# Kernel optimization log

Hardware: AMD Instinct MI355X
Metric: run time of the kernel (lower is better)

The kernel has to match this reference:

```python
import jax, jax.numpy as jnp
import numpy as np

T, H, NH, NKV, HD = 4096, 2048, 16, 2, 256
ROT = 64           # partial_rotary_factor 0.25 * head_dim 256
HALF = ROT // 2    # 32 == sum(mrope_section [11, 11, 10])
BASE = 10_000_000.0
EPS = 1e-6
SCALE = HD ** -0.5


def setup_inputs() -> dict:
    key = jax.random.key(0)
    ks = jax.random.split(key, 8)
    s = 0.02
    return {
        "positions": jnp.sort(jax.random.randint(ks[0], (3, T), 0, 4096), axis=-1),
        "hidden": jax.random.normal(ks[1], (T, H), jnp.float32),
        "Wq": jax.random.normal(ks[2], (H, NH * HD * 2), jnp.float32) * s,
        "Wk": jax.random.normal(ks[3], (H, NKV * HD), jnp.float32) * s,
        "Wv": jax.random.normal(ks[4], (H, NKV * HD), jnp.float32) * s,
        "Wo": jax.random.normal(ks[5], (NH * HD, H), jnp.float32) * s,
        "q_norm_w": jax.random.normal(ks[6], (HD,), jnp.float32) * 0.1,
        "k_norm_w": jax.random.normal(ks[7], (HD,), jnp.float32) * 0.1,
    }


def _rms(x, w):
    # GemmaRMSNorm: x / rms * (1 + w), per-head over last dim
    var = jnp.mean(x * x, axis=-1, keepdims=True)
    return x * jax.lax.rsqrt(var + EPS) * (1.0 + w)


def _rope_tables(positions):
    # interleaved MRoPE: freq j uses position axis j % 3 -> counts [11,11,10]
    inv_freq = BASE ** (-jnp.arange(0, ROT, 2, dtype=jnp.float32) / ROT)  # [HALF]
    axis = jnp.arange(HALF) % 3
    pos = positions[axis, :].astype(jnp.float32)   # [HALF, T]
    freqs = pos.T * inv_freq                       # [T, HALF]
    return jnp.cos(freqs), jnp.sin(freqs)


def _apply_rope(x, cos, sin):
    # x: [T, heads, HD]; rotate first ROT dims (neox half-split), rest pass through
    x1, x2 = x[..., :HALF], x[..., HALF:ROT]
    c, s = cos[:, None, :], sin[:, None, :]
    return jnp.concatenate([x1 * c - x2 * s, x2 * c + x1 * s, x[..., ROT:]], axis=-1)


def reference(positions, hidden, Wq, Wk, Wv, Wo, q_norm_w, k_norm_w):
    qg = (hidden @ Wq).reshape(T, NH, 2 * HD)
    q, gate = qg[..., :HD], qg[..., HD:]          # chunk(2, dim=-1)
    k = (hidden @ Wk).reshape(T, NKV, HD)
    v = (hidden @ Wv).reshape(T, NKV, HD)
    q = _rms(q, q_norm_w)
    k = _rms(k, k_norm_w)
    cos, sin = _rope_tables(positions)
    q = _apply_rope(q, cos, sin)
    k = _apply_rope(k, cos, sin)
    # GQA causal attention: group 16 Q heads over 2 KV heads
    g = NH // NKV
    q4 = q.reshape(T, NKV, g, HD)
    scores = jnp.einsum('qkgd,tkd->kgqt', q4, k) * SCALE   # [NKV, g, T, T]
    mask = jnp.tril(jnp.ones((T, T), dtype=bool))
    scores = jnp.where(mask[None, None], scores, -jnp.inf)
    probs = jax.nn.softmax(scores, axis=-1)
    o = jnp.einsum('kgqt,tkd->qkgd', probs, v).reshape(T, NH, HD)
    o = o * jax.nn.sigmoid(gate)                   # per-head output gating
    return o.reshape(T, NH * HD) @ Wo
```

## Files before the change

kernel.cpp:

```cpp
#include <hip/hip_runtime.h>
#include <hip/hip_bf16.h>


#define T_SZ 4096
#define H_SZ 2048
#define NH_SZ 16
#define NKV_SZ 2
#define HD_SZ 256
#define ATT_SCALE 0.0625f
#define SOFT_M 18.0f
#define EPS_ 1e-6f

typedef __attribute__((ext_vector_type(8))) short bf16x8;
typedef __attribute__((ext_vector_type(4))) float f32x4;

#define MFMA16(a, b, c) __builtin_amdgcn_mfma_f32_16x16x32_bf16((a), (b), (c), 0, 0, 0)

__device__ __forceinline__ void async16(const void* g, void* l) {
  __builtin_amdgcn_global_load_lds((const __attribute__((address_space(1))) void*)g,
                                   (__attribute__((address_space(3))) void*)l,
                                   16, 0, 0);
}

__device__ __forceinline__ float to_f(float x) { return x; }
__device__ __forceinline__ float to_f(__hip_bfloat16 x) { return __bfloat162float(x); }

union BfBits { __hip_bfloat16 h; unsigned short u; };

__device__ __forceinline__ unsigned short bf16_bits(__hip_bfloat16 h) {
  BfBits t; t.h = h; return t.u;
}

__device__ __forceinline__ unsigned pack_hilo(float v) {
  __hip_bfloat16 hi = __float2bfloat16(v);
  float rem = v - __bfloat162float(hi);
  __hip_bfloat16 lo = __float2bfloat16(rem);
  return (unsigned)bf16_bits(hi) | ((unsigned)bf16_bits(lo) << 16);
}

__global__ __launch_bounds__(256) void cast_f32_bf16(const float* __restrict__ in,
                                                     __hip_bfloat16* __restrict__ out,
                                                     int n4) {
  int i = blockIdx.x * 256 + threadIdx.x;
  if (i >= n4) return;
  float4 v = ((const float4*)in)[i];
  union { __hip_bfloat16 h[4]; uint2 u; } t;
  t.h[0] = __float2bfloat16(v.x);
  t.h[1] = __float2bfloat16(v.y);
  t.h[2] = __float2bfloat16(v.z);
  t.h[3] = __float2bfloat16(v.w);
  ((uint2*)out)[i] = t.u;
}

template <typename TIN>
__global__ __launch_bounds__(256) void transpose_cast(const TIN* __restrict__ in,
                                                      __hip_bfloat16* __restrict__ out,
                                                      int R, int C) {
  __shared__ TIN tile[32][33];
  int c0 = blockIdx.x * 32, r0 = blockIdx.y * 32;
  int tx = threadIdx.x & 31, ty = threadIdx.x >> 5;
#pragma unroll
  for (int i = 0; i < 32; i += 8)
    tile[ty + i][tx] = in[(long)(r0 + ty + i) * C + c0 + tx];
  __syncthreads();
#pragma unroll
  for (int i = 0; i < 32; i += 8)
    out[(long)(c0 + ty + i) * R + r0 + tx] = __float2bfloat16(to_f(tile[tx][ty + i]));
}

__global__ __launch_bounds__(256) void transpose_dup(const float* __restrict__ in,
                                                     unsigned* __restrict__ out,
                                                     int R, int C) {
  __shared__ float tile[32][33];
  int c0 = blockIdx.x * 32, r0 = blockIdx.y * 32;
  int tx = threadIdx.x & 31, ty = threadIdx.x >> 5;
#pragma unroll
  for (int i = 0; i < 32; i += 8)
    tile[ty + i][tx] = in[(long)(r0 + ty + i) * C + c0 + tx];
  __syncthreads();
#pragma unroll
  for (int i = 0; i < 32; i += 8) {
    unsigned short b = bf16_bits(__float2bfloat16(tile[tx][ty + i]));
    out[(long)(c0 + ty + i) * R + r0 + tx] = (unsigned)b | ((unsigned)b << 16);
  }
}

__global__ __launch_bounds__(512) void gemm_qg2(const __hip_bfloat16* __restrict__ A,
                                                const __hip_bfloat16* __restrict__ BT,
                                                float* __restrict__ qout,
                                                __hip_bfloat16* __restrict__ gate) {
  __shared__ __align__(16) __hip_bfloat16 As[4][8192];
  __shared__ __align__(16) __hip_bfloat16 Bs[4][8192];
  const int tid = threadIdx.x, wid = tid >> 6, lane = tid & 63;
  const int lo = lane & 15, quad = lane >> 4;
  const int wm = (wid >> 2) * 128, wn = (wid & 3) * 64;
  const int wg = blockIdx.x + blockIdx.y * 8;
  const int xcd = wg & 7, i_ = wg >> 3;
  const long n0 = (long)(xcd * 4 + (i_ & 3)) * 256;
  const long m0 = (long)(i_ >> 2) * 256;
  const int K = 2048;

  const int r0_ = tid >> 2;
  const int kc0 = (tid & 3) ^ ((tid >> 3) & 3);
  const __hip_bfloat16* sA0 = A + (m0 + r0_) * K + kc0 * 8;
  const __hip_bfloat16* sA1 = A + (m0 + r0_ + 128) * K + kc0 * 8;
  const __hip_bfloat16* sB0 = BT + (n0 + r0_) * K + kc0 * 8;
  const __hip_bfloat16* sB1 = BT + (n0 + r0_ + 128) * K + kc0 * 8;

  const int xq = (lo >> 1) & 3;
  const int aoff = (wm + lo) * 32 + ((quad ^ xq) * 8);
  const int boff = (wn + lo) * 32 + ((quad ^ xq) * 8);

  const f32x4 z4 = {0.f, 0.f, 0.f, 0.f};
  f32x4 acc[8][4];
#pragma unroll
  for (int fr = 0; fr < 8; ++fr)
#pragma unroll
    for (int fn = 0; fn < 4; ++fn) acc[fr][fn] = z4;

#define QG_STAGE(buf, kt) do {                                   \
    const int off_ = (kt) * 32;                                  \
    async16(sA0 + off_, &As[buf][tid * 8]);                      \
    async16(sA1 + off_, &As[buf][tid * 8 + 4096]);               \
    async16(sB0 + off_, &Bs[buf][tid * 8]);                      \
    async16(sB1 + off_, &Bs[buf][tid * 8 + 4096]);               \
  } while (0)

#define QG_COMPUTE(buf_) do {                                    \
    bf16x8 af[8], bq[4];                                         \
    _Pragma("unroll")                                            \
    for (int fr = 0; fr < 8; ++fr)                               \
      af[fr] = *(const bf16x8*)(&As[buf_][aoff + fr * 512]);     \
    _Pragma("unroll")                                            \
    for (int fn = 0; fn < 4; ++fn)                               \
      bq[fn] = *(const bf16x8*)(&Bs[buf_][boff + fn * 512]);     \
    __builtin_amdgcn_s_setprio(1);                               \
    _Pragma("unroll")                                            \
    for (int fr = 0; fr < 8; ++fr)                               \
      _Pragma("unroll")                                          \
      for (int fn = 0; fn < 4; ++fn)                             \
        acc[fr][fn] = MFMA16(af[fr], bq[fn], acc[fr][fn]);       \
    __builtin_amdgcn_s_setprio(0);                               \
  } while (0)

  QG_STAGE(0, 0); QG_STAGE(1, 1); QG_STAGE(2, 2);
  for (int kt = 0; kt < 61; ++kt) {
    asm volatile("s_waitcnt vmcnt(8)" ::: "memory");
    __builtin_amdgcn_s_barrier();
    __builtin_amdgcn_sched_barrier(0);
    QG_STAGE((kt + 3) & 3, kt + 3);
    __builtin_amdgcn_sched_barrier(0);
    QG_COMPUTE(kt & 3);
  }
  asm volatile("s_waitcnt vmcnt(8)" ::: "memory");
  __builtin_amdgcn_s_barrier();
  __builtin_amdgcn_sched_barrier(0);
  QG_COMPUTE(1);
  asm volatile("s_waitcnt vmcnt(4)" ::: "memory");
  __builtin_amdgcn_s_barrier();
  __builtin_amdgcn_sched_barrier(0);
  QG_COMPUTE(2);
  asm volatile("s_waitcnt vmcnt(0)" ::: "memory");
  __builtin_amdgcn_s_barrier();
  __builtin_amdgcn_sched_barrier(0);
  QG_COMPUTE(3);
#undef QG_STAGE
#undef QG_COMPUTE

#pragma unroll
  for (int fr = 0; fr < 8; ++fr)
#pragma unroll
    for (int fn = 0; fn < 4; ++fn)
#pragma unroll
      for (int rr = 0; rr < 4; ++rr) {
        long row = m0 + wm + fr * 16 + quad * 4 + rr;
        long col = n0 + wn + fn * 16 + lo;
        int head = (int)(col >> 9), c = (int)(col & 511);
        float v = acc[fr][fn][rr];
        if (c < 256)
          qout[(row * NH_SZ + head) * 256 + c] = v;
        else
          gate[(row * NH_SZ + head) * 256 + (c - 256)] = __float2bfloat16(v);
      }
}

__global__ __launch_bounds__(512) void gemm_out2(const __hip_bfloat16* __restrict__ A,
                                                 const __hip_bfloat16* __restrict__ BT,
                                                 float* __restrict__ C) {
  __shared__ __align__(16) __hip_bfloat16 As[4][8192];
  __shared__ __align__(16) __hip_bfloat16 Bs[4][4096];
  const int tid = threadIdx.x, wid = tid >> 6, lane = tid & 63;
  const int lo = lane & 15, quad = lane >> 4;
  const int wm = (wid >> 1) * 64, wn = (wid & 1) * 64;
  const int wg = blockIdx.x + blockIdx.y * 8;
  const int xcd = wg & 7, i_ = wg >> 3;
  const long n0 = (long)(xcd * 2 + (i_ & 1)) * 128;
  const long m0 = (long)(i_ >> 1) * 256;
  const long Kp = 8192;

  const int rA = tid >> 2, spx = (tid & 3) ^ ((tid >> 2) & 3);
  const __hip_bfloat16* sA0 = A + (m0 + rA) * Kp + spx * 8;
  const __hip_bfloat16* sA1 = A + (m0 + rA + 128) * Kp + spx * 8;
  const __hip_bfloat16* sB0 = BT + (n0 + rA) * Kp + spx * 8;

  const int xa = quad ^ (lo & 3);
  const int aoff = (wm + lo) * 32 + xa * 8;
  const int boff = (wn + lo) * 32 + xa * 8;

  const f32x4 z4 = {0.f, 0.f, 0.f, 0.f};
  f32x4 acc[4][4];
#pragma unroll
  for (int fr = 0; fr < 4; ++fr)
#pragma unroll
    for (int fn = 0; fn < 4; ++fn) acc[fr][fn] = z4;

#define GO_STAGE(buf, kt) do {                                   \
    const long off_ = (long)(kt) * 32;                           \
    async16(sA0 + off_, &As[buf][tid * 8]);                      \
    async16(sA1 + off_, &As[buf][tid * 8 + 4096]);               \
    async16(sB0 + off_, &Bs[buf][tid * 8]);                      \
  } while (0)

#define GO_COMPUTE(buf_) do {                                    \
    bf16x8 af[4], bq[4];                                         \
    _Pragma("unroll")                                            \
    for (int fr = 0; fr < 4; ++fr)                               \
      af[fr] = *(const bf16x8*)(&As[buf_][aoff + fr * 512]);     \
    _Pragma("unroll")                                            \
    for (int fn = 0; fn < 4; ++fn)                               \
      bq[fn] = *(const bf16x8*)(&Bs[buf_][boff + fn * 512]);     \
    __builtin_amdgcn_s_setprio(1);                               \
    _Pragma("unroll")                                            \
    for (int fr = 0; fr < 4; ++fr)                               \
      _Pragma("unroll")                                          \
      for (int fn = 0; fn < 4; ++fn)                             \
        acc[fr][fn] = MFMA16(af[fr], bq[fn], acc[fr][fn]);       \
    __builtin_amdgcn_s_setprio(0);                               \
  } while (0)

  GO_STAGE(0, 0); GO_STAGE(1, 1); GO_STAGE(2, 2);
  for (int kt = 0; kt < 253; ++kt) {
    asm volatile("s_waitcnt vmcnt(6)" ::: "memory");
    __builtin_amdgcn_s_barrier();
    __builtin_amdgcn_sched_barrier(0);
    GO_STAGE((kt + 3) & 3, kt + 3);
    __builtin_amdgcn_sched_barrier(0);
    GO_COMPUTE(kt & 3);
  }
  asm volatile("s_waitcnt vmcnt(6)" ::: "memory");
  __builtin_amdgcn_s_barrier();
  __builtin_amdgcn_sched_barrier(0);
  GO_COMPUTE(1);
  asm volatile("s_waitcnt vmcnt(3)" ::: "memory");
  __builtin_amdgcn_s_barrier();
  __builtin_amdgcn_sched_barrier(0);
  GO_COMPUTE(2);
  asm volatile("s_waitcnt vmcnt(0)" ::: "memory");
  __builtin_amdgcn_s_barrier();
  __builtin_amdgcn_sched_barrier(0);
  GO_COMPUTE(3);
#undef GO_STAGE
#undef GO_COMPUTE

#pragma unroll
  for (int fr = 0; fr < 4; ++fr)
#pragma unroll
    for (int fn = 0; fn < 4; ++fn)
#pragma unroll
      for (int rr = 0; rr < 4; ++rr) {
        long row = m0 + wm + fr * 16 + quad * 4 + rr;
        long col = n0 + wn + fn * 16 + lo;
        C[row * 2048 + col] = acc[fr][fn][rr];
      }
}

__global__ __launch_bounds__(256) void gemm_kv(const __hip_bfloat16* __restrict__ A,
                                               const __hip_bfloat16* __restrict__ BT,
                                               float* __restrict__ kf,
                                               __hip_bfloat16* __restrict__ vraw,
                                               int M, int N, int K) {
  __shared__ __align__(16) __hip_bfloat16 As[128 * 32];
  __shared__ __align__(16) __hip_bfloat16 Bs[128 * 32];
  const int tid = threadIdx.x;
  const int wid = tid >> 6, lane = tid & 63;
  const int lo = lane & 15, quad = lane >> 4;
  const int wq = blockIdx.x + blockIdx.y * 8;
  const int xcd = wq & 7, idx = wq >> 3;
  const long n0 = (long)xcd * 128;
  const long m0 = (long)idx * 128;
  const int wm = (wid >> 1) * 64, wn = (wid & 1) * 64;
  const f32x4 z4 = {0.f, 0.f, 0.f, 0.f};
  f32x4 acc[4][4];
#pragma unroll
  for (int i = 0; i < 4; ++i)
#pragma unroll
    for (int j = 0; j < 4; ++j) acc[i][j] = z4;

  const int cf0 = tid, cf1 = 256 + tid;
  const int r0_ = cf0 >> 2, c0_ = (cf0 & 3) * 8;
  const int r1_ = cf1 >> 2, c1_ = (cf1 & 3) * 8;
  const __hip_bfloat16* a0 = A + (m0 + r0_) * K + c0_;
  const __hip_bfloat16* a1 = A + (m0 + r1_) * K + c1_;
  const __hip_bfloat16* b0 = BT + (n0 + r0_) * K + c0_;
  const __hip_bfloat16* b1 = BT + (n0 + r1_) * K + c1_;

  for (int k0 = 0; k0 < K; k0 += 32) {
    async16(a0 + k0, As + cf0 * 8);
    async16(a1 + k0, As + cf1 * 8);
    async16(b0 + k0, Bs + cf0 * 8);
    async16(b1 + k0, Bs + cf1 * 8);
    __syncthreads();
    bf16x8 af[4], bfv[4];
#pragma unroll
    for (int i = 0; i < 4; ++i)
      af[i] = *(const bf16x8*)(As + (wm + i * 16 + lo) * 32 + quad * 8);
#pragma unroll
    for (int i = 0; i < 4; ++i)
      bfv[i] = *(const bf16x8*)(Bs + (wn + i * 16 + lo) * 32 + quad * 8);
#pragma unroll
    for (int i = 0; i < 4; ++i)
#pragma unroll
      for (int j = 0; j < 4; ++j) acc[i][j] = MFMA16(af[i], bfv[j], acc[i][j]);
    __syncthreads();
  }
#pragma unroll
  for (int i = 0; i < 4; ++i)
#pragma unroll
    for (int j = 0; j < 4; ++j)
#pragma unroll
      for (int r = 0; r < 4; ++r) {
        long row = m0 + wm + i * 16 + quad * 4 + r;
        long col = n0 + wn + j * 16 + lo;
        float v = acc[i][j][r];
        if (col < 512)
          kf[row * 512 + col] = v;
        else
          vraw[row * 512 + (col - 512)] = __float2bfloat16(v);
      }
}

__global__ __launch_bounds__(256) void v_swizzle(const __hip_bfloat16* __restrict__ vraw,
                                                 __hip_bfloat16* __restrict__ vsw) {
  const int ktt = blockIdx.x, kvh = blockIdx.y, tid = threadIdx.x;
  __shared__ __hip_bfloat16 L[64 * 264];
#pragma unroll
  for (int it = 0; it < 8; ++it) {
    int cf = it * 256 + tid;
    int kv = cf >> 5, d0 = (cf & 31) * 8;
    *(uint4*)&L[kv * 264 + d0] =
        *(const uint4*)&vraw[(((long)ktt * 64 + kv) * NKV_SZ + kvh) * 256 + d0];
  }
  __syncthreads();
#pragma unroll
  for (int it = 0; it < 8; ++it) {
    int cf = it * 256 + tid;
    int c = cf >> 8, d = cf & 255;
    union { __hip_bfloat16 h[8]; uint4 u; } t;
#pragma unroll
    for (int e = 0; e < 8; ++e) t.h[e] = L[(c * 8 + e) * 264 + d];
    *(uint4*)&vsw[((long)kvh * 64 + ktt) * 16384 + (long)(c * 256 + d) * 8] = t.u;
  }
}

__global__ __launch_bounds__(256) void norm_rope_wave(float* __restrict__ qbuf,
                                                      const float* __restrict__ kbuf,
                                                      __hip_bfloat16* __restrict__ ksw,
                                                      const int* __restrict__ pos,
                                                      const float* __restrict__ qw,
                                                      const float* __restrict__ kw) {
  const int id = blockIdx.x * 4 + (threadIdx.x >> 6);
  const int lane = threadIdx.x & 63;
  const int h = id % 18, t = id / 18;
  const bool isq = h < NH_SZ;
  const float* ptr = isq ? qbuf + ((long)t * NH_SZ + h) * 256
                         : kbuf + ((long)t * NKV_SZ + (h - NH_SZ)) * 256;
  const float* w = isq ? qw : kw;
  float4 v = *(const float4*)(ptr + lane * 4);
  float4 wv = *(const float4*)(w + lane * 4);
  float s2 = v.x * v.x + v.y * v.y + v.z * v.z + v.w * v.w;
#pragma unroll
  for (int o = 32; o > 0; o >>= 1) s2 += __shfl_xor(s2, o);
  float sc = rsqrtf(s2 * (1.0f / 256.0f) + EPS_);
  float n[4];
  n[0] = v.x * sc * (1.0f + wv.x);
  n[1] = v.y * sc * (1.0f + wv.y);
  n[2] = v.z * sc * (1.0f + wv.z);
  n[3] = v.w * sc * (1.0f + wv.w);
  float pr[4];
#pragma unroll
  for (int j = 0; j < 4; ++j) pr[j] = __shfl_xor(n[j], 8);
  float o4[4];
  if (lane < 16) {
    int base_i = (lane & 7) * 4;
#pragma unroll
    for (int j = 0; j < 4; ++j) {
      int i = base_i + j;
      float p = (float)pos[(i % 3) * T_SZ + t];
      float fr = p * exp2f((float)i * (-0.72667177075661f));
      float c, s;
      sincosf(fr, &s, &c);
      o4[j] = (lane < 8) ? n[j] * c - pr[j] * s : n[j] * c + pr[j] * s;
    }
  } else {
#pragma unroll
    for (int j = 0; j < 4; ++j) o4[j] = n[j];
  }
  if (isq) {
    uint4 u;
    u.x = pack_hilo(o4[0]); u.y = pack_hilo(o4[1]);
    u.z = pack_hilo(o4[2]); u.w = pack_hilo(o4[3]);
    *(uint4*)((unsigned*)qbuf + ((long)t * NH_SZ + h) * 256 + lane * 4) = u;
  } else {
    int kv = h - NH_SZ;
    long tt = t >> 5; int r = t & 31;
    int c = lane >> 1, e0 = (lane & 1) * 4;
    union { __hip_bfloat16 h4[4]; uint2 u; } kk;
#pragma unroll
    for (int j = 0; j < 4; ++j) kk.h4[j] = __float2bfloat16(o4[j]);
    *(uint2*)&ksw[(((long)kv * 128 + tt) * 32 + c) * 256 + r * 8 + e0] = kk.u;
  }
}

__global__ __launch_bounds__(256) void attn_kernel(unsigned* __restrict__ Qp,
                                                   const __hip_bfloat16* __restrict__ Ksw,
                                                   const __hip_bfloat16* __restrict__ Vsw,
                                                   const __hip_bfloat16* __restrict__ Gt) {
  const int w = blockIdx.x + blockIdx.y * 64;
  const int xcd = w & 7, j = w >> 3;
  const int h = xcd * 2 + (j & 1);
  const int qt = 63 - (j >> 1);
  const int kvh = h >> 3;
  const int tid = threadIdx.x, wid = tid >> 6, lane = tid & 63;
  const int lo = lane & 15, quad = lane >> 4;
  __shared__ __align__(16) __hip_bfloat16 Ks[32 * 256];
  __shared__ __align__(16) __hip_bfloat16 Vs[4 * 2048];
  __shared__ __align__(16) __hip_bfloat16 Ps[4][16 * 40];

  __hip_bfloat16* myP = &Ps[wid][0];
  const f32x4 z4 = {0.f, 0.f, 0.f, 0.f};
  const int nt = 2 * (qt + 1);

  bf16x8 qh[8], ql[8];
  {
    const unsigned* qp =
        Qp + ((long)(qt * 64 + wid * 16 + lo) * NH_SZ + h) * 256 + quad * 8;
#pragma unroll
    for (int kc = 0; kc < 8; ++kc) {
      uint4 p0 = *(const uint4*)(qp + kc * 32);
      uint4 p1 = *(const uint4*)(qp + kc * 32 + 4);
      bf16x8 a, b;
      a[0] = (short)(p0.x & 0xffff); b[0] = (short)(p0.x >> 16);
      a[1] = (short)(p0.y & 0xffff); b[1] = (short)(p0.y >> 16);
      a[2] = (short)(p0.z & 0xffff); b[2] = (short)(p0.z >> 16);
      a[3] = (short)(p0.w & 0xffff); b[3] = (short)(p0.w >> 16);
      a[4] = (short)(p1.x & 0xffff); b[4] = (short)(p1.x >> 16);
      a[5] = (short)(p1.y & 0xffff); b[5] = (short)(p1.y >> 16);
      a[6] = (short)(p1.z & 0xffff); b[6] = (short)(p1.z >> 16);
      a[7] = (short)(p1.w & 0xffff); b[7] = (short)(p1.w >> 16);
      qh[kc] = a; ql[kc] = b;
    }
  }

  f32x4 acc[16];
#pragma unroll
  for (int od = 0; od < 16; ++od) acc[od] = z4;
  float lsum[4];
#pragma unroll
  for (int r = 0; r < 4; ++r) lsum[r] = 0.f;

  const int qrow_g = qt * 64 + wid * 16 + quad * 4;
  const __hip_bfloat16* kbase = Ksw + (long)kvh * 1048576;
  const __hip_bfloat16* vbase = Vsw + (long)kvh * 1048576;

#pragma unroll
  for (int i = 0; i < 4; ++i) {
    int m = i * 4 + wid;
    async16(kbase + m * 512 + lane * 8, Ks + m * 512 + lane * 8);
    async16(vbase + m * 512 + lane * 8, Vs + m * 512 + lane * 8);
  }
  __syncthreads();

  for (int kt = 0; kt < nt; ++kt) {
    const bool skip = (kt == nt - 1) && (wid < 2);
    f32x4 s[2];
    s[0] = z4; s[1] = z4;
    if (!skip) {
      __builtin_amdgcn_s_setprio(1);
#pragma unroll
      for (int kc = 0; kc < 8; ++kc) {
        bf16x8 ah = qh[kc], al = ql[kc];
#pragma unroll
        for (int ni = 0; ni < 2; ++ni) {
          bf16x8 b = *(const bf16x8*)(Ks + (kc * 4 + quad) * 256 + (ni * 16 + lo) * 8);
          s[ni] = MFMA16(ah, b, s[ni]);
          s[ni] = MFMA16(al, b, s[ni]);
        }
      }
      __builtin_amdgcn_s_setprio(0);
    }
    __syncthreads();
    if (kt + 1 < nt) {
      const __hip_bfloat16* kb = kbase + (long)(kt + 1) * 8192;
#pragma unroll
      for (int i = 0; i < 4; ++i) {
        int m = i * 4 + wid;
        async16(kb + m * 512 + lane * 8, Ks + m * 512 + lane * 8);
      }
    }
    if (!skip) {
      float sv[2][4];
      if (kt >= nt - 2) {
#pragma unroll
        for (int ni = 0; ni < 2; ++ni) {
          int kcol = kt * 32 + ni * 16 + lo;
#pragma unroll
          for (int r = 0; r < 4; ++r) {
            float e = __expf(fmaf(s[ni][r], ATT_SCALE, -SOFT_M));
            sv[ni][r] = (kcol > qrow_g + r) ? 0.f : e;
          }
        }
      } else {
#pragma unroll
        for (int ni = 0; ni < 2; ++ni)
#pragma unroll
          for (int r = 0; r < 4; ++r)
            sv[ni][r] = __expf(fmaf(s[ni][r], ATT_SCALE, -SOFT_M));
      }
#pragma unroll
      for (int r = 0; r < 4; ++r) lsum[r] += sv[0][r] + sv[1][r];
#pragma unroll
      for (int ni = 0; ni < 2; ++ni)
#pragma unroll
        for (int r = 0; r < 4; ++r)
          myP[(quad * 4 + r) * 40 + ni * 16 + lo] = __float2bfloat16(sv[ni][r]);
      bf16x8 ap = *(const bf16x8*)(myP + lo * 40 + quad * 8);
      __builtin_amdgcn_s_setprio(1);
#pragma unroll
      for (int od = 0; od < 16; ++od) {
        bf16x8 bv = *(const bf16x8*)(Vs + quad * 2048 + (od * 16 + lo) * 8);
        acc[od] = MFMA16(ap, bv, acc[od]);
      }
      __builtin_amdgcn_s_setprio(0);
    }
    __syncthreads();
    if (kt + 1 < nt) {
      const __hip_bfloat16* vb = vbase + (long)(kt + 1) * 8192;
#pragma unroll
      for (int i = 0; i < 4; ++i) {
        int m = i * 4 + wid;
        async16(vb + m * 512 + lane * 8, Vs + m * 512 + lane * 8);
      }
    }
  }

  float l_r[4];
#pragma unroll
  for (int r = 0; r < 4; ++r) {
    float su = lsum[r];
#pragma unroll
    for (int off = 1; off < 16; off <<= 1) su += __shfl_xor(su, off);
    l_r[r] = su;
  }
#pragma unroll
  for (int od = 0; od < 16; ++od)
#pragma unroll
    for (int r = 0; r < 4; ++r) {
      int trow = qt * 64 + wid * 16 + quad * 4 + r;
      int col = od * 16 + lo;
      long idx = ((long)trow * NH_SZ + h) * 256 + col;
      float g = __bfloat162float(Gt[idx]);
      float sig = 1.0f / (1.0f + expf(-g));
      float v = (acc[od][r] / l_r[r]) * sig;
      Qp[idx] = pack_hilo(v);
    }
}

extern "C" void kernel_launch(void* const* d_in, const int* in_sizes, int n_in,
                              void* d_out, int out_size, void* d_ws, size_t ws_size,
                              hipStream_t stream) {
  (void)in_sizes; (void)n_in; (void)out_size; (void)ws_size;
  const int* positions = (const int*)d_in[0];
  const float* hidden = (const float*)d_in[1];
  const float* Wq = (const float*)d_in[2];
  const float* Wk = (const float*)d_in[3];
  const float* Wv = (const float*)d_in[4];
  const float* Wo = (const float*)d_in[5];
  const float* qw = (const float*)d_in[6];
  const float* kw = (const float*)d_in[7];
  float* out = (float*)d_out;
  char* ws = (char*)d_ws;

  __hip_bfloat16* hid  = (__hip_bfloat16*)(ws + 0);
  __hip_bfloat16* WqT  = (__hip_bfloat16*)(ws + 16777216);
  __hip_bfloat16* WkT  = (__hip_bfloat16*)(ws + 50331648);
  __hip_bfloat16* WvT  = (__hip_bfloat16*)(ws + 52428800);
  float*          qf   = (float*)(ws + 54525952);
  __hip_bfloat16* gate = (__hip_bfloat16*)(ws + 121634816);
  float*          kf   = (float*)(ws + 155189248);
  __hip_bfloat16* vraw = (__hip_bfloat16*)(ws + 163577856);
  __hip_bfloat16* Ksw  = WkT;
  __hip_bfloat16* Vsw  = hid;
  unsigned*       Wo2  = (unsigned*)WqT;
  unsigned* qpk = (unsigned*)qf;

  cast_f32_bf16<<<dim3(8192), dim3(256), 0, stream>>>(hidden, hid, 2097152);
  transpose_cast<float><<<dim3(256, 64), dim3(256), 0, stream>>>(Wq, WqT, 2048, 8192);
  transpose_cast<float><<<dim3(16, 64), dim3(256), 0, stream>>>(Wk, WkT, 2048, 512);
  transpose_cast<float><<<dim3(16, 64), dim3(256), 0, stream>>>(Wv, WvT, 2048, 512);
  gemm_qg2<<<dim3(8, 64), dim3(512), 0, stream>>>(hid, WqT, qf, gate);
  gemm_kv<<<dim3(8, 32), dim3(256), 0, stream>>>(hid, WkT, kf, vraw, 4096, 1024, 2048);
  v_swizzle<<<dim3(64, 2), dim3(256), 0, stream>>>(vraw, Vsw);
  norm_rope_wave<<<dim3(18432), dim3(256), 0, stream>>>(qf, kf, Ksw, positions, qw, kw);
  attn_kernel<<<dim3(64, 16), dim3(256), 0, stream>>>(qpk, Ksw, Vsw, gate);
  transpose_dup<<<dim3(64, 128), dim3(256), 0, stream>>>(Wo, Wo2, 4096, 2048);
  gemm_out2<<<dim3(8, 32), dim3(512), 0, stream>>>((const __hip_bfloat16*)qpk,
                                                   (const __hip_bfloat16*)Wo2, out);
}
```

Baseline: 861.9 us.

## Deepen out-proj GEMM K-step to 64 with 3-stage buffering and new swizzle

The output projection GEMM now loads two 32-wide K slices per pipeline stage, using three stages instead of four single-slice stages. This halves the number of barriers and waitcnt synchronisations per K and issues more loads per stage. The LDS swizzle is changed to key on (row>>1)&3 to reduce bank conflicts. The cost is higher LDS usage, which may limit occupancy, and fewer stages of prefetch depth in steps.

```diff
diff --git a/kernel.cpp b/kernel.cpp
--- a/kernel.cpp
+++ b/kernel.cpp
@@ -187,8 +187,8 @@
 __global__ __launch_bounds__(512) void gemm_out2(const __hip_bfloat16* __restrict__ A,
                                                  const __hip_bfloat16* __restrict__ BT,
                                                  float* __restrict__ C) {
-  __shared__ __align__(16) __hip_bfloat16 As[4][8192];
-  __shared__ __align__(16) __hip_bfloat16 Bs[4][4096];
+  __shared__ __align__(16) __hip_bfloat16 As[3][2][8192];
+  __shared__ __align__(16) __hip_bfloat16 Bs[3][2][4096];
   const int tid = threadIdx.x, wid = tid >> 6, lane = tid & 63;
   const int lo = lane & 15, quad = lane >> 4;
   const int wm = (wid >> 1) * 64, wn = (wid & 1) * 64;
@@ -198,14 +198,15 @@
   const long m0 = (long)(i_ >> 1) * 256;
   const long Kp = 8192;
 
-  const int rA = tid >> 2, spx = (tid & 3) ^ ((tid >> 2) & 3);
-  const __hip_bfloat16* sA0 = A + (m0 + rA) * Kp + spx * 8;
-  const __hip_bfloat16* sA1 = A + (m0 + rA + 128) * Kp + spx * 8;
-  const __hip_bfloat16* sB0 = BT + (n0 + rA) * Kp + spx * 8;
-
-  const int xa = quad ^ (lo & 3);
-  const int aoff = (wm + lo) * 32 + xa * 8;
-  const int boff = (wn + lo) * 32 + xa * 8;
+  const int r0_ = tid >> 2;
+  const int kc0 = (tid & 3) ^ ((tid >> 3) & 3);
+  const __hip_bfloat16* sA0 = A + (m0 + r0_) * Kp + kc0 * 8;
+  const __hip_bfloat16* sA1 = A + (m0 + r0_ + 128) * Kp + kc0 * 8;
+  const __hip_bfloat16* sB0 = BT + (n0 + r0_) * Kp + kc0 * 8;
+
+  const int xq = (lo >> 1) & 3;
+  const int aoff = (wm + lo) * 32 + ((quad ^ xq) * 8);
+  const int boff = (wn + lo) * 32 + ((quad ^ xq) * 8);
 
   const f32x4 z4 = {0.f, 0.f, 0.f, 0.f};
   f32x4 acc[4][4];
@@ -215,50 +216,52 @@
     for (int fn = 0; fn < 4; ++fn) acc[fr][fn] = z4;
 
 #define GO_STAGE(buf, kt) do {                                   \
-    const long off_ = (long)(kt) * 32;                           \
-    async16(sA0 + off_, &As[buf][tid * 8]);                      \
-    async16(sA1 + off_, &As[buf][tid * 8 + 4096]);               \
-    async16(sB0 + off_, &Bs[buf][tid * 8]);                      \
+    const long off_ = (long)(kt) * 64;                           \
+    async16(sA0 + off_,      &As[buf][0][tid * 8]);              \
+    async16(sA1 + off_,      &As[buf][0][tid * 8 + 4096]);       \
+    async16(sA0 + off_ + 32, &As[buf][1][tid * 8]);              \
+    async16(sA1 + off_ + 32, &As[buf][1][tid * 8 + 4096]);       \
+    async16(sB0 + off_,      &Bs[buf][0][tid * 8]);              \
+    async16(sB0 + off_ + 32, &Bs[buf][1][tid * 8]);              \
   } while (0)
 
 #define GO_COMPUTE(buf_) do {                                    \
-    bf16x8 af[4], bq[4];                                         \
     _Pragma("unroll")                                            \
-    for (int fr = 0; fr < 4; ++fr)                               \
-      af[fr] = *(const bf16x8*)(&As[buf_][aoff + fr * 512]);     \
-    _Pragma("unroll")                                            \
-    for (int fn = 0; fn < 4; ++fn)                               \
-      bq[fn] = *(const bf16x8*)(&Bs[buf_][boff + fn * 512]);     \
-    __builtin_amdgcn_s_setprio(1);                               \
-    _Pragma("unroll")                                            \
-    for (int fr = 0; fr < 4; ++fr)                               \
+    for (int ks = 0; ks < 2; ++ks) {                             \
+      bf16x8 af[4], bq[4];                                       \
+      _Pragma("unroll")                                          \
+      for (int fr = 0; fr < 4; ++fr)                             \
+        af[fr] = *(const bf16x8*)(&As[buf_][ks][aoff + fr * 512]); \
       _Pragma("unroll")                                          \
       for (int fn = 0; fn < 4; ++fn)                             \
-        acc[fr][fn] = MFMA16(af[fr], bq[fn], acc[fr][fn]);       \
-    __builtin_amdgcn_s_setprio(0);                               \
+        bq[fn] = *(const bf16x8*)(&Bs[buf_][ks][boff + fn * 512]); \
+      __builtin_amdgcn_s_setprio(1);                             \
+      _Pragma("unroll")                                          \
+      for (int fr = 0; fr < 4; ++fr)                             \
+        _Pragma("unroll")                                        \
+        for (int fn = 0; fn < 4; ++fn)                           \
+          acc[fr][fn] = MFMA16(af[fr], bq[fn], acc[fr][fn]);     \
+      __builtin_amdgcn_s_setprio(0);                             \
+    }                                                            \
   } while (0)
 
-  GO_STAGE(0, 0); GO_STAGE(1, 1); GO_STAGE(2, 2);
-  for (int kt = 0; kt < 253; ++kt) {
+  GO_STAGE(0, 0); GO_STAGE(1, 1);
+  for (int kt = 0; kt < 126; ++kt) {
     asm volatile("s_waitcnt vmcnt(6)" ::: "memory");
     __builtin_amdgcn_s_barrier();
     __builtin_amdgcn_sched_barrier(0);
-    GO_STAGE((kt + 3) & 3, kt + 3);
+    GO_STAGE((kt + 2) % 3, kt + 2);
     __builtin_amdgcn_sched_barrier(0);
-    GO_COMPUTE(kt & 3);
+    GO_COMPUTE(kt % 3);
   }
   asm volatile("s_waitcnt vmcnt(6)" ::: "memory");
   __builtin_amdgcn_s_barrier();
   __builtin_amdgcn_sched_barrier(0);
-  GO_COMPUTE(1);
-  asm volatile("s_waitcnt vmcnt(3)" ::: "memory");
-  __builtin_amdgcn_s_barrier();
-  __builtin_amdgcn_sched_barrier(0);
-  GO_COMPUTE(2);
+  GO_COMPUTE(0);
   asm volatile("s_waitcnt vmcnt(0)" ::: "memory");
   __builtin_amdgcn_s_barrier();
   __builtin_amdgcn_sched_barrier(0);
-  GO_COMPUTE(3);
+  GO_COMPUTE(1);
 #undef GO_STAGE
 #undef GO_COMPUTE
 
```

Measured after the change: 828.2 us. 3.9% less time.
